# Performance work log

Measured on AMD Instinct MI355X. Metric: run time of the kernel, lower is better.

The kernel has to match this reference:

```python
import jax, jax.numpy as jnp
import numpy as np


def setup_inputs() -> dict:
    key = jax.random.key(0)
    ks = jax.random.split(key, 8)
    R, N = 8192, 4096  # rows, set size (n == m required by the module's mm shapes)
    X = jax.random.normal(ks[0], (R, N), dtype=jnp.float32)
    Y = jax.random.normal(ks[1], (R, N), dtype=jnp.float32)
    # scalar parameters, init uniform(0,1) as in _init_weights
    l_xx = jax.random.uniform(ks[2], (1,), dtype=jnp.float32)
    l_yy = jax.random.uniform(ks[3], (1,), dtype=jnp.float32)
    g_xx = jax.random.uniform(ks[4], (1,), dtype=jnp.float32)
    g_xy = jax.random.uniform(ks[5], (1,), dtype=jnp.float32)
    g_yx = jax.random.uniform(ks[6], (1,), dtype=jnp.float32)
    g_yy = jax.random.uniform(ks[7], (1,), dtype=jnp.float32)
    return {"X": X, "Y": Y, "l_xx": l_xx, "l_yy": l_yy,
            "g_xx": g_xx, "g_xy": g_xy, "g_yx": g_yx, "g_yy": g_yy}


def reference(X, Y, l_xx, l_yy, g_xx, g_xy, g_yx, g_yy):
    n = X.shape[-1]
    m = Y.shape[-1]
    # theta_xx = I_n * l_xx + ones(n,n) * g_xx ; theta_yy analogous
    theta_xx = jnp.eye(n, dtype=X.dtype) * l_xx + jnp.ones((n, n), dtype=X.dtype) * g_xx
    theta_yy = jnp.eye(m, dtype=X.dtype) * l_yy + jnp.ones((m, m), dtype=X.dtype) * g_yy
    theta_xy = jnp.ones((m, n), dtype=X.dtype) * g_xy  # maps Y-features -> ... (requires m == n)
    theta_yx = jnp.ones((n, m), dtype=X.dtype) * g_yx
    o_x = X @ theta_xx + Y @ theta_yx
    o_y = Y @ theta_yy + X @ theta_xy
    return (o_x, o_y)
```

## Files before the change

### kernel.cpp

```cpp
#include <hip/hip_runtime.h>


constexpr int N_COLS = 4096;

typedef float v4f __attribute__((ext_vector_type(4)));

__global__ __launch_bounds__(1024, 8) void pequinn_rowaffine(
    const float* __restrict__ X, const float* __restrict__ Y,
    const float* __restrict__ p_lxx, const float* __restrict__ p_lyy,
    const float* __restrict__ p_gxx, const float* __restrict__ p_gxy,
    const float* __restrict__ p_gyx, const float* __restrict__ p_gyy,
    float* __restrict__ o_x, float* __restrict__ o_y)
{
    const int row = blockIdx.x;
    const int tid = threadIdx.x;
    const size_t base = (size_t)row * N_COLS;

    const v4f* Xr = (const v4f*)(X + base);
    const v4f* Yr = (const v4f*)(Y + base);

    const v4f xv = __builtin_nontemporal_load(Xr + tid);
    const v4f yv = __builtin_nontemporal_load(Yr + tid);

    float sx = (xv.x + xv.y) + (xv.z + xv.w);
    float sy = (yv.x + yv.y) + (yv.z + yv.w);

#pragma unroll
    for (int off = 32; off > 0; off >>= 1) {
        sx += __shfl_down(sx, off, 64);
        sy += __shfl_down(sy, off, 64);
    }

    __shared__ float ssx[16], ssy[16];
    const int wave = tid >> 6;
    const int lane = tid & 63;
    if (lane == 0) { ssx[wave] = sx; ssy[wave] = sy; }
    __syncthreads();

    float SX = 0.f, SY = 0.f;
#pragma unroll
    for (int i = 0; i < 16; ++i) {
        SX += ssx[i];
        SY += ssy[i];
    }

    const float lxx = p_lxx[0], lyy = p_lyy[0];
    const float gxx = p_gxx[0], gxy = p_gxy[0];
    const float gyx = p_gyx[0], gyy = p_gyy[0];

    const float bx = gxx * SX + gyx * SY;
    const float by = gyy * SY + gxy * SX;

    v4f ox, oy;
    ox.x = fmaf(lxx, xv.x, bx);
    ox.y = fmaf(lxx, xv.y, bx);
    ox.z = fmaf(lxx, xv.z, bx);
    ox.w = fmaf(lxx, xv.w, bx);
    oy.x = fmaf(lyy, yv.x, by);
    oy.y = fmaf(lyy, yv.y, by);
    oy.z = fmaf(lyy, yv.z, by);
    oy.w = fmaf(lyy, yv.w, by);

    __builtin_nontemporal_store(ox, (v4f*)(o_x + base) + tid);
    __builtin_nontemporal_store(oy, (v4f*)(o_y + base) + tid);
}

extern "C" void kernel_launch(void* const* d_in, const int* in_sizes, int n_in,
                              void* d_out, int out_size, void* d_ws, size_t ws_size,
                              hipStream_t stream) {
    const float* X    = (const float*)d_in[0];
    const float* Y    = (const float*)d_in[1];
    const float* lxx  = (const float*)d_in[2];
    const float* lyy  = (const float*)d_in[3];
    const float* gxx  = (const float*)d_in[4];
    const float* gxy  = (const float*)d_in[5];
    const float* gyx  = (const float*)d_in[6];
    const float* gyy  = (const float*)d_in[7];

    const int R = in_sizes[0] / N_COLS;
    float* o_x = (float*)d_out;
    float* o_y = (float*)d_out + (size_t)R * N_COLS;

    pequinn_rowaffine<<<R, 1024, 0, stream>>>(X, Y, lxx, lyy, gxx, gxy, gyx, gyy,
                                              o_x, o_y);
}
```

Baseline: 424.7 us.

## Assign one wavefront per row and drop the block-level reduction

```diff
diff --git a/kernel.cpp b/kernel.cpp
--- a/kernel.cpp
+++ b/kernel.cpp
@@ -2,67 +2,72 @@
 
 
 constexpr int N_COLS = 4096;
+constexpr int V4_PER_LANE = N_COLS / 4 / 64;
 
 typedef float v4f __attribute__((ext_vector_type(4)));
 
-__global__ __launch_bounds__(1024, 8) void pequinn_rowaffine(
+__global__ __launch_bounds__(256, 4) void pequinn_waverow(
     const float* __restrict__ X, const float* __restrict__ Y,
     const float* __restrict__ p_lxx, const float* __restrict__ p_lyy,
     const float* __restrict__ p_gxx, const float* __restrict__ p_gxy,
     const float* __restrict__ p_gyx, const float* __restrict__ p_gyy,
     float* __restrict__ o_x, float* __restrict__ o_y)
 {
-    const int row = blockIdx.x;
-    const int tid = threadIdx.x;
+    const int wave = threadIdx.x >> 6;
+    const int lane = threadIdx.x & 63;
+    const int row  = blockIdx.x * 4 + wave;
     const size_t base = (size_t)row * N_COLS;
 
     const v4f* Xr = (const v4f*)(X + base);
     const v4f* Yr = (const v4f*)(Y + base);
 
-    const v4f xv = __builtin_nontemporal_load(Xr + tid);
-    const v4f yv = __builtin_nontemporal_load(Yr + tid);
-
-    float sx = (xv.x + xv.y) + (xv.z + xv.w);
-    float sy = (yv.x + yv.y) + (yv.z + yv.w);
+    float sx = 0.f, sy = 0.f;
+#pragma unroll
+    for (int i = 0; i < V4_PER_LANE; ++i) {
+        const v4f x = Xr[lane + 64 * i];
+        sx += (x.x + x.y) + (x.z + x.w);
+    }
+#pragma unroll
+    for (int i = 0; i < V4_PER_LANE; ++i) {
+        const v4f y = Yr[lane + 64 * i];
+        sy += (y.x + y.y) + (y.z + y.w);
+    }
 
 #pragma unroll
-    for (int off = 32; off > 0; off >>= 1) {
-        sx += __shfl_down(sx, off, 64);
-        sy += __shfl_down(sy, off, 64);
-    }
-
-    __shared__ float ssx[16], ssy[16];
-    const int wave = tid >> 6;
-    const int lane = tid & 63;
-    if (lane == 0) { ssx[wave] = sx; ssy[wave] = sy; }
-    __syncthreads();
-
-    float SX = 0.f, SY = 0.f;
-#pragma unroll
-    for (int i = 0; i < 16; ++i) {
-        SX += ssx[i];
-        SY += ssy[i];
+    for (int off = 1; off < 64; off <<= 1) {
+        sx += __shfl_xor(sx, off, 64);
+        sy += __shfl_xor(sy, off, 64);
     }
 
     const float lxx = p_lxx[0], lyy = p_lyy[0];
     const float gxx = p_gxx[0], gxy = p_gxy[0];
     const float gyx = p_gyx[0], gyy = p_gyy[0];
 
-    const float bx = gxx * SX + gyx * SY;
-    const float by = gyy * SY + gxy * SX;
+    const float bx = gxx * sx + gyx * sy;
+    const float by = gyy * sy + gxy * sx;
 
-    v4f ox, oy;
-    ox.x = fmaf(lxx, xv.x, bx);
-    ox.y = fmaf(lxx, xv.y, bx);
-    ox.z = fmaf(lxx, xv.z, bx);
-    ox.w = fmaf(lxx, xv.w, bx);
-    oy.x = fmaf(lyy, yv.x, by);
-    oy.y = fmaf(lyy, yv.y, by);
-    oy.z = fmaf(lyy, yv.z, by);
-    oy.w = fmaf(lyy, yv.w, by);
-
-    __builtin_nontemporal_store(ox, (v4f*)(o_x + base) + tid);
-    __builtin_nontemporal_store(oy, (v4f*)(o_y + base) + tid);
+    v4f* Ox = (v4f*)(o_x + base);
+    v4f* Oy = (v4f*)(o_y + base);
+#pragma unroll
+    for (int i = 0; i < V4_PER_LANE; ++i) {
+        const v4f x = Xr[lane + 64 * i];
+        v4f ox;
+        ox.x = fmaf(lxx, x.x, bx);
+        ox.y = fmaf(lxx, x.y, bx);
+        ox.z = fmaf(lxx, x.z, bx);
+        ox.w = fmaf(lxx, x.w, bx);
+        __builtin_nontemporal_store(ox, Ox + lane + 64 * i);
+    }
+#pragma unroll
+    for (int i = 0; i < V4_PER_LANE; ++i) {
+        const v4f y = Yr[lane + 64 * i];
+        v4f oy;
+        oy.x = fmaf(lyy, y.x, by);
+        oy.y = fmaf(lyy, y.y, by);
+        oy.z = fmaf(lyy, y.z, by);
+        oy.w = fmaf(lyy, y.w, by);
+        __builtin_nontemporal_store(oy, Oy + lane + 64 * i);
+    }
 }
 
 extern "C" void kernel_launch(void* const* d_in, const int* in_sizes, int n_in,
@@ -81,6 +86,6 @@
     float* o_x = (float*)d_out;
     float* o_y = (float*)d_out + (size_t)R * N_COLS;
 
-    pequinn_rowaffine<<<R, 1024, 0, stream>>>(X, Y, lxx, lyy, gxx, gxy, gyx, gyy,
-                                              o_x, o_y);
+    pequinn_waverow<<<R / 4, 256, 0, stream>>>(X, Y, lxx, lyy, gxx, gxy, gyx, gyy,
+                                               o_x, o_y);
 }
```

New measurement: 459.3 us. +8.2%, slower.
